# Kernel optimization log

Measured on AMD Instinct MI355X. Metric: run time of the kernel, lower is better.

## Reference

```python
import jax, jax.numpy as jnp
import numpy as np

NUM_HEADS = 16
ROPE_BASE = 10000.0


def _rope_cos_sin(seq_len, head_dim, dtype):
    inv_freq = 1.0 / (ROPE_BASE ** (jnp.arange(0, head_dim, 2, dtype=jnp.float32) / head_dim))
    t = jnp.arange(seq_len, dtype=jnp.float32)
    freqs = jnp.einsum('i,j->ij', t, inv_freq)          # [S, hd/2]
    emb = jnp.concatenate([freqs, freqs], axis=-1)      # [S, hd]
    return jnp.cos(emb).astype(dtype), jnp.sin(emb).astype(dtype)


def _rotate_half(x):
    x1, x2 = jnp.split(x, 2, axis=-1)
    return jnp.concatenate([-x2, x1], axis=-1)


def setup_inputs() -> dict:
    key = jax.random.key(0)
    k1, k2, k3 = jax.random.split(key, 3)
    B, S, D = 2, 2048, 2048
    x = jax.random.normal(k1, (B, S, D), dtype=jnp.float32)
    w_qkv = jax.random.normal(k2, (D, 3 * D), dtype=jnp.float32) * (D ** -0.5)
    w_out = jax.random.normal(k3, (D, D), dtype=jnp.float32) * (D ** -0.5)
    return {"x": x, "w_qkv": w_qkv, "w_out": w_out}


def reference(x, w_qkv, w_out):
    B, S, D = x.shape
    H = NUM_HEADS
    hd = D // H
    scale = hd ** -0.5

    qkv = jnp.einsum('bsd,de->bse', x, w_qkv)            # [B,S,3D]
    q, k, v = jnp.split(qkv, 3, axis=-1)
    # -> [B,H,S,hd]
    q = q.reshape(B, S, H, hd).transpose(0, 2, 1, 3)
    k = k.reshape(B, S, H, hd).transpose(0, 2, 1, 3)
    v = v.reshape(B, S, H, hd).transpose(0, 2, 1, 3)

    cos, sin = _rope_cos_sin(S, hd, x.dtype)             # [S,hd]
    cos = cos[None, None]                                # [1,1,S,hd]
    sin = sin[None, None]
    q = q * cos + _rotate_half(q) * sin
    k = k * cos + _rotate_half(k) * sin

    scores = jnp.einsum('bhqd,bhkd->bhqk', q, k) * scale  # [B,H,S,S]
    attn = jax.nn.softmax(scores, axis=-1)                # non-causal: no mask
    out = jnp.einsum('bhqk,bhkd->bhqd', attn, v)          # [B,H,S,hd]
    out = out.transpose(0, 2, 1, 3).reshape(B, S, D)
    out = jnp.einsum('bsd,de->bse', out, w_out)
    return out
```

## Files before the change

### kernel.cpp

```cpp
#include <hip/hip_runtime.h>
#include <hip/hip_bf16.h>

typedef __hip_bfloat16 bf16_t;
typedef __bf16 bf16x8 __attribute__((ext_vector_type(8)));
typedef float floatx4 __attribute__((ext_vector_type(4)));

#define DEVINL __device__ __forceinline__

DEVINL floatx4 mfma16(bf16x8 a, bf16x8 b, floatx4 c) {
  return __builtin_amdgcn_mfma_f32_16x16x32_bf16(a, b, c, 0, 0, 0);
}

DEVINL void gload_lds16(const bf16_t* gp, bf16_t* lp) {
  __builtin_amdgcn_global_load_lds(
      (const __attribute__((address_space(1))) unsigned int*)gp,
      (__attribute__((address_space(3))) unsigned int*)lp, 16, 0, 0);
}

template <class CT> DEVINL CT cvtC(float f);
template <> DEVINL bf16_t cvtC<bf16_t>(float f) { return __float2bfloat16(f); }
template <> DEVINL float cvtC<float>(float f) { return f; }

DEVINL unsigned int pack_bf2(float a, float b) {
  union { bf16_t h; unsigned short s; } ua, ub;
  ua.h = __float2bfloat16(a);
  ub.h = __float2bfloat16(b);
  return (unsigned int)ua.s | ((unsigned int)ub.s << 16);
}

__global__ void convert_f32_bf16(const float* __restrict__ in,
                                 bf16_t* __restrict__ out) {
  size_t i = ((size_t)blockIdx.x * 256 + threadIdx.x) * 8;
  floatx4 a = *(const floatx4*)(in + i);
  floatx4 b = *(const floatx4*)(in + i + 4);
  bf16x8 r;
#pragma unroll
  for (int j = 0; j < 4; j++) r[j] = (__bf16)a[j];
#pragma unroll
  for (int j = 0; j < 4; j++) r[4 + j] = (__bf16)b[j];
  *(bf16x8*)(out + i) = r;
}

template <bool SPLITV, class CT>
__global__ __launch_bounds__(512, 2) void gemm256(
    const bf16_t* __restrict__ A, const bf16_t* __restrict__ BT,
    CT* __restrict__ C, bf16_t* __restrict__ VTout, int M, int N, int CN,
    int K) {
  extern __shared__ __align__(16) char smem[];
  bf16_t* a_lds = (bf16_t*)smem;
  bf16_t* b_lds = a_lds + 32768;

  const int tid = threadIdx.x;
  const int w = tid >> 6;
  const int lane = tid & 63;
  const int quad = lane >> 4;
  const int l16 = lane & 15;
  const int wm = w >> 2, wn = w & 3;

  const int cpx = (int)gridDim.x >> 3;
  const int wgid = ((int)blockIdx.x & 7) * cpx + ((int)blockIdx.x >> 3);
  const int nym = M >> 8;
  const int row0 = (wgid % nym) * 256;
  const int col0 = (wgid / nym) * 256;

  floatx4 acc[2][2][4][2] = {};
  bf16x8 af[4][2], bfr[2][2];

  const bf16_t* agA = A + (size_t)(row0 + w * 16 + l16) * K + quad * 8;
  const bf16_t* agB = BT + (size_t)(col0 + w * 16 + l16) * K + quad * 8;
  const size_t rK = (size_t)128 * K;

#define STG_A(bb, rp, tt)                                                  \
  {                                                                        \
    _Pragma("unroll") for (int kc = 0; kc < 2; kc++)                       \
        gload_lds16(agA + (rp) * rK + (tt) * 64 + kc * 32,                 \
                    a_lds + (bb) * 16384 + ((rp) * 8 + w) * 1024 + kc * 512); \
  }
#define STG_B(bb, cp, tt)                                                  \
  {                                                                        \
    _Pragma("unroll") for (int kc = 0; kc < 2; kc++)                       \
        gload_lds16(agB + (cp) * rK + (tt) * 64 + kc * 32,                 \
                    b_lds + (bb) * 16384 + ((cp) * 8 + w) * 1024 + kc * 512); \
  }
#define LDA(cb, rp)                                                        \
  {                                                                        \
    _Pragma("unroll") for (int m = 0; m < 4; m++)                          \
        _Pragma("unroll") for (int kc = 0; kc < 2; kc++)                   \
            af[m][kc] = *(const bf16x8*)(a_lds + (cb) * 16384 +            \
                                         ((rp) * 8 + wm * 4 + m) * 1024 +  \
                                         kc * 512 + lane * 8);             \
  }
#define LDB(cb, cp)                                                        \
  {                                                                        \
    _Pragma("unroll") for (int n = 0; n < 2; n++)                          \
        _Pragma("unroll") for (int kc = 0; kc < 2; kc++)                   \
            bfr[n][kc] = *(const bf16x8*)(b_lds + (cb) * 16384 +           \
                                          ((cp) * 8 + wn * 2 + n) * 1024 + \
                                          kc * 512 + lane * 8);            \
  }
#define MM(rp, cp)                                                         \
  {                                                                        \
    __builtin_amdgcn_s_setprio(1);                                         \
    _Pragma("unroll") for (int kc = 0; kc < 2; kc++)                       \
        _Pragma("unroll") for (int m = 0; m < 4; m++)                      \
            _Pragma("unroll") for (int n = 0; n < 2; n++)                  \
                acc[rp][cp][m][n] =                                        \
                    mfma16(af[m][kc], bfr[n][kc], acc[rp][cp][m][n]);      \
    __builtin_amdgcn_s_setprio(0);                                         \
  }
#define BAR()                         \
  {                                   \
    __builtin_amdgcn_s_barrier();     \
    __builtin_amdgcn_sched_barrier(0); \
  }
#define VM(n)                                              \
  {                                                        \
    asm volatile("s_waitcnt vmcnt(" #n ")" ::: "memory");  \
    __builtin_amdgcn_sched_barrier(0);                     \
  }

#define TILE(tt, cb, nb, DOSTG, V0m, V1m, V3m)             \
  {                                                        \
     LDA(cb, 0); LDB(cb, 0);                         \
    if (DOSTG) { STG_A(nb, 0, (tt) + 1); STG_B(nb, 0, (tt) + 1); } \
    V0m BAR(); MM(0, 0); BAR();                            \
     LDB(cb, 1);                                     \
    if (DOSTG) STG_B(nb, 1, (tt) + 1);                     \
    V1m BAR(); MM(0, 1); BAR();                            \
     LDA(cb, 1);                                     \
    if (DOSTG) STG_A(nb, 1, (tt) + 1);                     \
    BAR(); MM(1, 1); BAR();                                \
     LDB(cb, 0);                                     \
    V3m BAR(); MM(1, 0); BAR();                            \
  }

  STG_A(0, 0, 0); STG_B(0, 0, 0); STG_B(0, 1, 0); STG_A(0, 1, 0);
  VM(4);
  __builtin_amdgcn_s_barrier();
  __builtin_amdgcn_sched_barrier(0);

  const int nt = K >> 6;
  for (int t = 0; t < nt - 2; t += 2) {
    TILE(t, 0, 1, 1, VM(6);, VM(6);, VM(4);)
    TILE(t + 1, 1, 0, 1, VM(6);, VM(6);, VM(4);)
  }
  TILE(nt - 2, 0, 1, 1, VM(6);, VM(6);, VM(4);)
  TILE(nt - 1, 1, 0, 0, VM(2);, VM(0);, )

#undef TILE
#undef VM
#undef BAR
#undef MM
#undef LDB
#undef LDA
#undef STG_B
#undef STG_A

  if (!SPLITV || col0 < 4096) {
#pragma unroll
    for (int rp = 0; rp < 2; rp++)
#pragma unroll
      for (int cp = 0; cp < 2; cp++)
#pragma unroll
        for (int m = 0; m < 4; m++)
#pragma unroll
          for (int n = 0; n < 2; n++)
#pragma unroll
            for (int r = 0; r < 4; r++) {
              int row = row0 + rp * 128 + wm * 64 + m * 16 + quad * 4 + r;
              int col = col0 + cp * 128 + wn * 32 + n * 16 + l16;
              C[(size_t)row * CN + col] = cvtC<CT>(acc[rp][cp][m][n][r]);
            }
  } else {
    const int b = row0 >> 11;
    const int s0 = row0 & 2047;
    struct __align__(8) bf4 { bf16_t v[4]; };
#pragma unroll
    for (int cp = 0; cp < 2; cp++) {
      const int h = ((col0 - 4096) >> 7) + cp;
      bf16_t* vt = VTout + (size_t)(b * 16 + h) * 128 * 2048;
#pragma unroll
      for (int rp = 0; rp < 2; rp++)
#pragma unroll
        for (int m = 0; m < 4; m++)
#pragma unroll
          for (int n = 0; n < 2; n++) {
            int d = wn * 32 + n * 16 + l16;
            int s = s0 + rp * 128 + wm * 64 + m * 16 + quad * 4;
            bf4 o;
#pragma unroll
            for (int r = 0; r < 4; r++)
              o.v[r] = __float2bfloat16(acc[rp][cp][m][n][r]);
            *(bf4*)(vt + (size_t)d * 2048 + s) = o;
          }
    }
  }
}

template <bool SPLITV, class CT>
__global__ __launch_bounds__(512, 2) void gemm128(
    const bf16_t* __restrict__ A, const bf16_t* __restrict__ BT,
    CT* __restrict__ C, bf16_t* __restrict__ VTout, int M, int N, int CN,
    int K) {
  extern __shared__ __align__(16) char smem[];
  bf16_t* a_lds = (bf16_t*)smem;
  bf16_t* b_lds = a_lds + 24576;

  const int tid = threadIdx.x;
  const int w = tid >> 6;
  const int lane = tid & 63;
  const int quad = lane >> 4;
  const int l16 = lane & 15;
  const int wm = w >> 2, wn = w & 3;

  const int cpx = (int)gridDim.x >> 3;
  const int wgid = ((int)blockIdx.x & 7) * cpx + ((int)blockIdx.x >> 3);
  const int nym = M >> 7;
  const int row0 = (wgid % nym) * 128;
  const int col0 = (wgid / nym) * 256;

  floatx4 acc[4][4] = {};
  bf16x8 af[4][2], bfr[2][2];

  const int nfE = (w >> 1) * 4 + (w & 1);
  const bf16_t* agA = A + (size_t)(row0 + w * 16 + l16) * K + quad * 8;
  const bf16_t* agB = BT + (size_t)(col0 + nfE * 16 + l16) * K + quad * 8;

#define STG_A(sb, tt)                                                      \
  {                                                                        \
    _Pragma("unroll") for (int kc = 0; kc < 2; kc++)                       \
        gload_lds16(agA + (tt) * 64 + kc * 32,                             \
                    a_lds + (sb) * 8192 + w * 1024 + kc * 512);            \
  }
#define STG_BE(sb, tt)                                                     \
  {                                                                        \
    _Pragma("unroll") for (int kc = 0; kc < 2; kc++)                       \
        gload_lds16(agB + (tt) * 64 + kc * 32,                             \
                    b_lds + (sb) * 16384 + nfE * 1024 + kc * 512);         \
  }
#define STG_BO(sb, tt)                                                     \
  {                                                                        \
    _Pragma("unroll") for (int kc = 0; kc < 2; kc++)                       \
        gload_lds16(agB + (size_t)32 * K + (tt) * 64 + kc * 32,            \
                    b_lds + (sb) * 16384 + (nfE + 2) * 1024 + kc * 512);   \
  }
#define LDA(cb)                                                            \
  {                                                                        \
    _Pragma("unroll") for (int m = 0; m < 4; m++)                          \
        _Pragma("unroll") for (int kc = 0; kc < 2; kc++)                   \
            af[m][kc] = *(const bf16x8*)(a_lds + (cb) * 8192 +             \
                                         (wm * 4 + m) * 1024 + kc * 512 +  \
                                         lane * 8);                        \
  }
#define LDB(cb, h)                                                         \
  {                                                                        \
    _Pragma("unroll") for (int jj = 0; jj < 2; jj++)                       \
        _Pragma("unroll") for (int kc = 0; kc < 2; kc++)                   \
            bfr[jj][kc] = *(const bf16x8*)(b_lds + (cb) * 16384 +          \
                                           (wn * 4 + 2 * (h) + jj) * 1024 + \
                                           kc * 512 + lane * 8);           \
  }
#define MM(h)                                                              \
  {                                                                        \
    __builtin_amdgcn_s_setprio(1);                                         \
    _Pragma("unroll") for (int kc = 0; kc < 2; kc++)                       \
        _Pragma("unroll") for (int m = 0; m < 4; m++)                      \
            _Pragma("unroll") for (int jj = 0; jj < 2; jj++)               \
                acc[m][2 * (h) + jj] = mfma16(af[m][kc], bfr[jj][kc],      \
                                              acc[m][2 * (h) + jj]);       \
    __builtin_amdgcn_s_setprio(0);                                         \
  }
#define BAR() __builtin_amdgcn_s_barrier();
#define VM(n) asm volatile("s_waitcnt vmcnt(" #n ")" ::: "memory");
#define LGK() asm volatile("s_waitcnt lgkmcnt(0)" ::: "memory");

#define TILE(tt, cb, sb, DOSTG, V0m, V1m)                  \
  {                                                        \
     LDA(cb); LDB(cb, 0);                            \
    if (DOSTG) { STG_A(sb, (tt) + 2); STG_BE(sb, (tt) + 2); } \
    V0m BAR(); LGK(); MM(0); BAR();                        \
     LDB(cb, 1);                                     \
    if (DOSTG) { STG_BO(sb, (tt) + 2); }                   \
    V1m BAR(); LGK(); MM(1); BAR();                        \
  }

  STG_A(0, 0); STG_BE(0, 0); STG_BO(0, 0);
  STG_A(1, 1); STG_BE(1, 1); STG_BO(1, 1);
  VM(8);
  __builtin_amdgcn_s_barrier();

  const int nt = K >> 6;
  for (int t = 0; t < nt - 2; t += 3) {
    TILE(t, 0, 2, 1, VM(10);, VM(8);)
    TILE(t + 1, 1, 0, 1, VM(10);, VM(8);)
    TILE(t + 2, 2, 1, 1, VM(10);, VM(8);)
  }
  TILE(nt - 2, 0, 0, 0, VM(6);, VM(2);)
  TILE(nt - 1, 1, 0, 0, VM(0);, )

#undef TILE
#undef LGK
#undef VM
#undef BAR
#undef MM
#undef LDB
#undef LDA
#undef STG_BO
#undef STG_BE
#undef STG_A

  if (!SPLITV || col0 < 4096) {
#pragma unroll
    for (int m = 0; m < 4; m++)
#pragma unroll
      for (int n = 0; n < 4; n++)
#pragma unroll
        for (int r = 0; r < 4; r++) {
          int row = row0 + wm * 64 + m * 16 + quad * 4 + r;
          int col = col0 + wn * 64 + n * 16 + l16;
          C[(size_t)row * CN + col] = cvtC<CT>(acc[m][n][r]);
        }
  } else {
    const int b = row0 >> 11;
    const int s0 = row0 & 2047;
    const int h = ((col0 - 4096) >> 7) + (wn >> 1);
    bf16_t* vt = VTout + (size_t)(b * 16 + h) * 128 * 2048;
    struct __align__(8) bf4 { bf16_t v[4]; };
#pragma unroll
    for (int m = 0; m < 4; m++)
#pragma unroll
      for (int n = 0; n < 4; n++) {
        int d = (wn & 1) * 64 + n * 16 + l16;
        int s = s0 + wm * 64 + m * 16 + quad * 4;
        bf4 o;
#pragma unroll
        for (int r = 0; r < 4; r++) o.v[r] = __float2bfloat16(acc[m][n][r]);
        *(bf4*)(vt + (size_t)d * 2048 + s) = o;
      }
  }
}

__global__ void transposecvt(const float* __restrict__ in,
                             bf16_t* __restrict__ out, int M, int N) {
  __shared__ bf16_t tile[32][33];
  int n0 = blockIdx.x * 32, m0 = blockIdx.y * 32;
  tile[threadIdx.y][threadIdx.x] =
      __float2bfloat16(in[(size_t)(m0 + threadIdx.y) * N + n0 + threadIdx.x]);
  __syncthreads();
  out[(size_t)(n0 + threadIdx.y) * M + m0 + threadIdx.x] =
      tile[threadIdx.x][threadIdx.y];
}

__global__ void rope_qk(bf16_t* __restrict__ qkv) {
  struct __align__(8) bf4 { bf16_t v[4]; };
  int t = blockIdx.x * 256 + threadIdx.x;
  int dc = t & 15;
  int s = (t >> 4) & 2047;
  int h = (t >> 15) & 15;
  int b = t >> 19;
  int d = dc * 4;
  size_t base = ((size_t)(b * 2048 + s) * 2) * 2048 + h * 128;
  bf4 ql = *(const bf4*)(qkv + base + d);
  bf4 qh = *(const bf4*)(qkv + base + d + 64);
  bf4 kl = *(const bf4*)(qkv + base + 2048 + d);
  bf4 kh = *(const bf4*)(qkv + base + 2048 + d + 64);
  bf4 oql, oqh, okl, okh;
  const float scale = 0.08838834764831845f;
#pragma unroll
  for (int i = 0; i < 4; i++) {
    int j = d + i;
    float fr = (float)s * exp2f((float)j * -0.20762050593045858f);
    float c, sn;
    __sincosf(fr, &sn, &c);
    float qlo = __bfloat162float(ql.v[i]), qhi = __bfloat162float(qh.v[i]);
    float klo = __bfloat162float(kl.v[i]), khi = __bfloat162float(kh.v[i]);
    oql.v[i] = __float2bfloat16((qlo * c - qhi * sn) * scale);
    oqh.v[i] = __float2bfloat16((qhi * c + qlo * sn) * scale);
    okl.v[i] = __float2bfloat16(klo * c - khi * sn);
    okh.v[i] = __float2bfloat16(khi * c + klo * sn);
  }
  *(bf4*)(qkv + base + d) = oql;
  *(bf4*)(qkv + base + d + 64) = oqh;
  *(bf4*)(qkv + base + 2048 + d) = okl;
  *(bf4*)(qkv + base + 2048 + d + 64) = okh;
}

__global__ __launch_bounds__(256, 2) void flash_attn(
    const bf16_t* __restrict__ qkv, const bf16_t* __restrict__ VT,
    bf16_t* __restrict__ Out) {
  const int S = 2048;
  const int RS = 4096;
  const int tid = threadIdx.x;
  const int wave = tid >> 6;
  const int lane = tid & 63;
  const int quad = lane >> 4;
  const int l16 = lane & 15;

  const int bh = blockIdx.y;
  const int q0 = blockIdx.x * 128;
  const int b = bh >> 4, h = bh & 15;

  const bf16_t* Qb = qkv + (size_t)b * S * RS + h * 128;
  const bf16_t* Kb = Qb + 2048;
  const bf16_t* Vb = VT + (size_t)bh * 128 * S;

  __shared__ __align__(16) bf16_t k_lds[16384];
  __shared__ __align__(16) bf16_t v_lds[16384];

  bf16x8 qf[2][4];
#pragma unroll
  for (int qn = 0; qn < 2; qn++)
#pragma unroll
    for (int ks = 0; ks < 4; ks++)
      qf[qn][ks] = *(const bf16x8*)(
          Qb + (size_t)(q0 + wave * 32 + qn * 16 + l16) * RS + ks * 32 +
          quad * 8);

  floatx4 o_acc[2][8] = {};
  float l_part[2] = {0.f, 0.f};

  const int sA = l16 + 32 * (quad & 1);
  const int sB = sA + 16;
  const bool hi = quad >= 2;

  for (int kt = 0; kt < S / 128; kt++) {
    const int kk0 = kt * 128;
#pragma unroll
    for (int t = 0; t < 2; t++) {
      int mt = wave * 2 + t;
#pragma unroll
      for (int ks = 0; ks < 4; ks++) {
        gload_lds16(Kb + (size_t)(kk0 + mt * 16 + l16) * RS + ks * 32 + quad * 8,
                    k_lds + mt * 2048 + ks * 512);
        gload_lds16(Vb + (size_t)(mt * 16 + l16) * S + kk0 + ks * 32 + quad * 8,
                    v_lds + mt * 2048 + ks * 512);
      }
    }
    __syncthreads();

    floatx4 s_acc[2][8] = {};
    __builtin_amdgcn_s_setprio(1);
#pragma unroll
    for (int ks = 0; ks < 4; ks++)
#pragma unroll
      for (int mt = 0; mt < 8; mt++) {
        bf16x8 kf = *(const bf16x8*)(k_lds + mt * 2048 + ks * 512 + lane * 8);
        s_acc[0][mt] = mfma16(kf, qf[0][ks], s_acc[0][mt]);
        s_acc[1][mt] = mfma16(kf, qf[1][ks], s_acc[1][mt]);
      }
    __builtin_amdgcn_s_setprio(0);

    unsigned int p01[2][8], p23[2][8];
#pragma unroll
    for (int qn = 0; qn < 2; qn++)
#pragma unroll
      for (int mt = 0; mt < 8; mt++) {
        float e0 = __expf(s_acc[qn][mt][0]);
        float e1 = __expf(s_acc[qn][mt][1]);
        float e2 = __expf(s_acc[qn][mt][2]);
        float e3 = __expf(s_acc[qn][mt][3]);
        l_part[qn] += (e0 + e1) + (e2 + e3);
        p01[qn][mt] = pack_bf2(e0, e1);
        p23[qn][mt] = pack_bf2(e2, e3);
      }

#pragma unroll
    for (int kc = 0; kc < 4; kc++) {
      bf16x8 vf[8];
#pragma unroll
      for (int dt = 0; dt < 8; dt++)
        vf[dt] = *(const bf16x8*)(v_lds + dt * 2048 + kc * 512 + lane * 8);
#pragma unroll
      for (int qn = 0; qn < 2; qn++) {
        unsigned int a0 = __shfl(p01[qn][2 * kc], sA);
        unsigned int b0 = __shfl(p01[qn][2 * kc + 1], sA);
        unsigned int a1 = __shfl(p23[qn][2 * kc], sA);
        unsigned int b1 = __shfl(p23[qn][2 * kc + 1], sA);
        unsigned int a2 = __shfl(p01[qn][2 * kc], sB);
        unsigned int b2 = __shfl(p01[qn][2 * kc + 1], sB);
        unsigned int a3 = __shfl(p23[qn][2 * kc], sB);
        unsigned int b3 = __shfl(p23[qn][2 * kc + 1], sB);
        union { unsigned int u[4]; bf16x8 v; } bp;
        bp.u[0] = hi ? b0 : a0;
        bp.u[1] = hi ? b1 : a1;
        bp.u[2] = hi ? b2 : a2;
        bp.u[3] = hi ? b3 : a3;
        __builtin_amdgcn_s_setprio(1);
#pragma unroll
        for (int dt = 0; dt < 8; dt++)
          o_acc[qn][dt] = mfma16(vf[dt], bp.v, o_acc[qn][dt]);
        __builtin_amdgcn_s_setprio(0);
      }
    }
    __syncthreads();
  }

#pragma unroll
  for (int qn = 0; qn < 2; qn++) {
    l_part[qn] += __shfl_xor(l_part[qn], 16);
    l_part[qn] += __shfl_xor(l_part[qn], 32);
  }

  struct __align__(8) bf4 { bf16_t v[4]; };
#pragma unroll
  for (int qn = 0; qn < 2; qn++) {
    float inv = 1.f / l_part[qn];
    size_t s = q0 + wave * 32 + qn * 16 + l16;
#pragma unroll
    for (int dt = 0; dt < 8; dt++) {
      bf4 o;
#pragma unroll
      for (int r = 0; r < 4; r++)
        o.v[r] = __float2bfloat16(o_acc[qn][dt][r] * inv);
      *(bf4*)(Out + ((size_t)b * S + s) * 2048 + h * 128 + dt * 16 + quad * 4) = o;
    }
  }
}

extern "C" void kernel_launch(void* const* d_in, const int* in_sizes, int n_in,
                              void* d_out, int out_size, void* d_ws,
                              size_t ws_size, hipStream_t stream) {
  const float* x = (const float*)d_in[0];
  const float* w_qkv = (const float*)d_in[1];
  const float* w_out = (const float*)d_in[2];
  float* out = (float*)d_out;
  char* ws = (char*)d_ws;

  const int B = 2, S = 2048, D = 2048;
  bf16_t* qkv2 = (bf16_t*)(ws);
  bf16_t* wqkvT = (bf16_t*)(ws + (size_t)B * S * 2 * D * 2);
  bf16_t* xbf = (bf16_t*)(ws + (size_t)B * S * 2 * D * 2 + (size_t)3 * D * D * 2);
  bf16_t* VT = (bf16_t*)(ws + (size_t)B * S * 2 * D * 2 + (size_t)3 * D * D * 2 +
                         (size_t)B * S * D * 2);
  bf16_t* attn = wqkvT;
  bf16_t* woutT = qkv2;

  hipFuncSetAttribute(reinterpret_cast<const void*>(&gemm256<true, bf16_t>),
                      hipFuncAttributeMaxDynamicSharedMemorySize, 131072);
  hipFuncSetAttribute(reinterpret_cast<const void*>(&gemm128<false, float>),
                      hipFuncAttributeMaxDynamicSharedMemorySize, 147456);

  dim3 b32(32, 32);
  convert_f32_bf16<<<(B * S * D) / 2048, 256, 0, stream>>>(x, xbf);
  transposecvt<<<dim3(3 * D / 32, D / 32), b32, 0, stream>>>(w_qkv, wqkvT, D, 3 * D);
  gemm256<true, bf16_t><<<(B * S / 256) * (3 * D / 256), 512, 131072, stream>>>(
      xbf, wqkvT, qkv2, VT, B * S, 3 * D, 2 * D, D);
  rope_qk<<<4096, 256, 0, stream>>>(qkv2);
  flash_attn<<<dim3(S / 128, B * 16), 256, 0, stream>>>(qkv2, VT, attn);
  transposecvt<<<dim3(D / 32, D / 32), b32, 0, stream>>>(w_out, woutT, D, D);
  gemm128<false, float><<<(B * S / 128) * (D / 256), 512, 147456, stream>>>(
      attn, woutT, out, nullptr, B * S, D, D, D);
}
```

Measured before the change: 439.5 us.

## Keep both B fragments in registers and vectorize weight transpose-convert

The 256-tile GEMM now holds separate register fragments for both B column halves, so the fourth sub-step reuses the fragment loaded in the first instead of reloading it from LDS. This removes one round of LDS reads per K tile at the cost of more VGPRs, which may affect occupancy or cause spills. Separately, the weight transpose-and-convert kernel now works on 64x64 tiles with 256 threads, float4 global loads and 8-byte bf16 stores, instead of 32x32 tiles with scalar accesses, to raise memory throughput for the two weight conversions.

```diff
diff --git a/kernel.cpp b/kernel.cpp
--- a/kernel.cpp
+++ b/kernel.cpp
@@ -64,7 +64,7 @@
   const int col0 = (wgid / nym) * 256;
 
   floatx4 acc[2][2][4][2] = {};
-  bf16x8 af[4][2], bfr[2][2];
+  bf16x8 af[4][2], bfr[2][2][2];
 
   const bf16_t* agA = A + (size_t)(row0 + w * 16 + l16) * K + quad * 8;
   const bf16_t* agB = BT + (size_t)(col0 + w * 16 + l16) * K + quad * 8;
@@ -94,7 +94,7 @@
   {                                                                        \
     _Pragma("unroll") for (int n = 0; n < 2; n++)                          \
         _Pragma("unroll") for (int kc = 0; kc < 2; kc++)                   \
-            bfr[n][kc] = *(const bf16x8*)(b_lds + (cb) * 16384 +           \
+            bfr[cp][n][kc] = *(const bf16x8*)(b_lds + (cb) * 16384 +       \
                                           ((cp) * 8 + wn * 2 + n) * 1024 + \
                                           kc * 512 + lane * 8);            \
   }
@@ -105,7 +105,7 @@
         _Pragma("unroll") for (int m = 0; m < 4; m++)                      \
             _Pragma("unroll") for (int n = 0; n < 2; n++)                  \
                 acc[rp][cp][m][n] =                                        \
-                    mfma16(af[m][kc], bfr[n][kc], acc[rp][cp][m][n]);      \
+                    mfma16(af[m][kc], bfr[cp][n][kc], acc[rp][cp][m][n]);  \
     __builtin_amdgcn_s_setprio(0);                                         \
   }
 #define BAR()                         \
@@ -130,7 +130,7 @@
      LDA(cb, 1);                                     \
     if (DOSTG) STG_A(nb, 1, (tt) + 1);                     \
     BAR(); MM(1, 1); BAR();                                \
-     LDB(cb, 0);                                     \
+                \
     V3m BAR(); MM(1, 0); BAR();                            \
   }
 
@@ -342,13 +342,28 @@
 
 __global__ void transposecvt(const float* __restrict__ in,
                              bf16_t* __restrict__ out, int M, int N) {
-  __shared__ bf16_t tile[32][33];
-  int n0 = blockIdx.x * 32, m0 = blockIdx.y * 32;
-  tile[threadIdx.y][threadIdx.x] =
-      __float2bfloat16(in[(size_t)(m0 + threadIdx.y) * N + n0 + threadIdx.x]);
+  __shared__ bf16_t tile[64][65];
+  const int t = threadIdx.x;
+  const int tx = t & 15;
+  const int tr = t >> 4;
+  const int n0 = blockIdx.x * 64, m0 = blockIdx.y * 64;
+#pragma unroll
+  for (int i = 0; i < 4; i++) {
+    floatx4 v =
+        *(const floatx4*)(in + (size_t)(m0 + tr * 4 + i) * N + n0 + tx * 4);
+#pragma unroll
+    for (int j = 0; j < 4; j++)
+      tile[tr * 4 + i][tx * 4 + j] = __float2bfloat16(v[j]);
+  }
   __syncthreads();
-  out[(size_t)(n0 + threadIdx.y) * M + m0 + threadIdx.x] =
-      tile[threadIdx.x][threadIdx.y];
+  struct __align__(8) bf4 { bf16_t v[4]; };
+#pragma unroll
+  for (int i = 0; i < 4; i++) {
+    bf4 o;
+#pragma unroll
+    for (int j = 0; j < 4; j++) o.v[j] = tile[tx * 4 + j][tr * 4 + i];
+    *(bf4*)(out + (size_t)(n0 + tr * 4 + i) * M + m0 + tx * 4) = o;
+  }
 }
 
 __global__ void rope_qk(bf16_t* __restrict__ qkv) {
@@ -540,14 +555,13 @@
   hipFuncSetAttribute(reinterpret_cast<const void*>(&gemm128<false, float>),
                       hipFuncAttributeMaxDynamicSharedMemorySize, 147456);
 
-  dim3 b32(32, 32);
   convert_f32_bf16<<<(B * S * D) / 2048, 256, 0, stream>>>(x, xbf);
-  transposecvt<<<dim3(3 * D / 32, D / 32), b32, 0, stream>>>(w_qkv, wqkvT, D, 3 * D);
+  transposecvt<<<dim3(3 * D / 64, D / 64), 256, 0, stream>>>(w_qkv, wqkvT, D, 3 * D);
   gemm256<true, bf16_t><<<(B * S / 256) * (3 * D / 256), 512, 131072, stream>>>(
       xbf, wqkvT, qkv2, VT, B * S, 3 * D, 2 * D, D);
   rope_qk<<<4096, 256, 0, stream>>>(qkv2);
   flash_attn<<<dim3(S / 128, B * 16), 256, 0, stream>>>(qkv2, VT, attn);
-  transposecvt<<<dim3(D / 32, D / 32), b32, 0, stream>>>(w_out, woutT, D, D);
+  transposecvt<<<dim3(D / 64, D / 64), 256, 0, stream>>>(w_out, woutT, D, D);
   gemm128<false, float><<<(B * S / 128) * (D / 256), 512, 147456, stream>>>(
       attn, woutT, out, nullptr, B * S, D, D, D);
 }
```

New measurement: 438.4 us. Within noise of the previous version (-0.2%).
